# Kernel tuning notes

Hardware: AMD Instinct MI355X
Metric: run time of the kernel (lower is better)

## Reference

```python
import math
import jax, jax.numpy as jnp
import numpy as np

DEPTH, EMB, HEADS = 6, 768, 12
B, N = 2, 2048
LN_EPS = 1e-6


def _get_attention_slopes(n):
    def p2(n):
        start = 2 ** (-2 ** (-(math.log2(n) - 3)))
        return [start * start ** i for i in range(n)]
    if math.log2(n).is_integer():
        return p2(n)
    c = 2 ** math.floor(math.log2(n))
    return p2(c) + _get_attention_slopes(2 * c)[0::2][: n - c]


def layer_norm(x, scale, bias):
    m = jnp.mean(x, axis=-1, keepdims=True)
    v = jnp.var(x, axis=-1, keepdims=True)
    return (x - m) * jax.lax.rsqrt(v + LN_EPS) * scale + bias


def setup_inputs() -> dict:
    key = jax.random.key(0)
    ks = jax.random.split(key, 6)
    s = 0.02
    return {
        "x": jax.random.normal(ks[0], (B, N, EMB), jnp.float32),
        "wqkv": jax.random.normal(ks[1], (DEPTH, EMB, 3 * EMB), jnp.float32) * s,
        "bqkv": jnp.zeros((DEPTH, 3 * EMB), jnp.float32),
        "wo": jax.random.normal(ks[2], (DEPTH, EMB, EMB), jnp.float32) * s,
        "bo": jnp.zeros((DEPTH, EMB), jnp.float32),
        "ln1s": jnp.ones((DEPTH, EMB), jnp.float32),
        "ln1b": jnp.zeros((DEPTH, EMB), jnp.float32),
        "ln2s": jnp.ones((DEPTH, EMB), jnp.float32),
        "ln2b": jnp.zeros((DEPTH, EMB), jnp.float32),
        "w1": jax.random.normal(ks[3], (DEPTH, EMB, 4 * EMB), jnp.float32) * s,
        "w2": jax.random.normal(ks[4], (DEPTH, 4 * EMB, EMB), jnp.float32) * s,
        "lnfs": jnp.ones((EMB,), jnp.float32),
        "lnfb": jnp.zeros((EMB,), jnp.float32),
    }


def reference(x, wqkv, bqkv, wo, bo, ln1s, ln1b, ln2s, ln2b, w1, w2, lnfs, lnfb):
    Bx, n, E = x.shape
    H = HEADS
    Dh = E // H
    scale = Dh ** -0.5
    slopes = jnp.asarray(_get_attention_slopes(H), dtype=x.dtype)  # [H]
    # ALiBi-style bias: slope[h] * key-position (absolute), per source code
    pos_bias = slopes[:, None, None] * jnp.arange(n, dtype=x.dtype)[None, None, :]  # [H,1,n]
    causal = jnp.tril(jnp.ones((n, n), bool))
    big_neg = jnp.finfo(x.dtype).min

    def block(h, p):
        Wqkv, Bqkv, Wo, Bo, L1s, L1b, L2s, L2b, W1, W2 = p
        y = layer_norm(h, L1s, L1b)
        qkv = y @ Wqkv + Bqkv  # [B,n,3E]
        q, k, v = jnp.split(qkv, 3, axis=-1)
        mh = lambda t: t.reshape(Bx, n, H, Dh).transpose(0, 2, 1, 3)  # b h n d
        q, k, v = mh(q), mh(k), mh(v)
        att = jnp.einsum("bhnd,bhmd->bhnm", q, k) * scale + pos_bias[None]
        att = jnp.where(causal, att, big_neg)
        att = jax.nn.softmax(att, axis=-1)
        o = jnp.einsum("bhnm,bhmd->bhnd", att, v)
        o = o.transpose(0, 2, 1, 3).reshape(Bx, n, E) @ Wo + Bo
        h = h + o
        y = layer_norm(h, L2s, L2b)
        y = jax.nn.gelu(y @ W1) @ W2  # fc1 (no bias) -> gelu -> fc2 (no bias)
        return h + y, None

    h, _ = jax.lax.scan(block, x, (wqkv, bqkv, wo, bo, ln1s, ln1b, ln2s, ln2b, w1, w2))
    return layer_norm(h, lnfs, lnfb)
```

## Files before the change

### kernel.cpp

```cpp
#include <hip/hip_runtime.h>
#include <hip/hip_bf16.h>
#include <stdint.h>


typedef __bf16 bf16_t;
typedef __bf16 bf16x8 __attribute__((ext_vector_type(8)));
typedef __bf16 bf16x4 __attribute__((ext_vector_type(4)));
typedef float f32x4 __attribute__((ext_vector_type(4)));

#define EMB   768
#define NSEQ  2048
#define BATCH 2
#define NHEAD 12
#define NDEPTH 6
#define MROWS (BATCH * NSEQ)

__constant__ float c_slopes[NHEAD] = {
    0.5f, 0.25f, 0.125f, 0.0625f, 0.03125f, 0.015625f, 0.0078125f, 0.00390625f,
    0.7071067811865476f, 0.3535533905932738f, 0.1767766952966369f, 0.08838834764831845f};

__global__ void detect_kernel(const void* __restrict__ lnfs, int* __restrict__ flag) {
  if (threadIdx.x == 0 && blockIdx.x == 0) {
    uint32_t u = *(const uint32_t*)lnfs;
    *flag = (u == 0x3F800000u) ? 0 : 1;
  }
}

__global__ void fill_one_kernel(bf16_t* __restrict__ o, int n) {
  int i = blockIdx.x * blockDim.x + threadIdx.x;
  if (i < n) o[i] = (bf16_t)1.0f;
}

__global__ void cast_kernel(const void* __restrict__ x_, float* __restrict__ h, int n,
                            const int* __restrict__ flagp) {
  const int flag = *flagp;
  int i = blockIdx.x * blockDim.x + threadIdx.x;
  if (i < n) h[i] = flag ? (float)((const bf16_t*)x_)[i] : ((const float*)x_)[i];
}

template <int FINAL>
__global__ __launch_bounds__(256) void ln_kernel(const float* __restrict__ x,
                                                 const void* __restrict__ sc_,
                                                 const void* __restrict__ bi_,
                                                 size_t eoff, void* __restrict__ y_,
                                                 const int* __restrict__ flagp) {
  const int flag = *flagp;
  const int widx = blockIdx.x * 4 + (threadIdx.x >> 6);
  const int lane = threadIdx.x & 63;
  const float* row = x + (size_t)widx * EMB;
  float v[12];
  float sum = 0.f, ss = 0.f;
#pragma unroll
  for (int i = 0; i < 12; ++i) {
    float t = row[lane + i * 64];
    v[i] = t; sum += t; ss += t * t;
  }
#pragma unroll
  for (int m = 1; m < 64; m <<= 1) {
    sum += __shfl_xor(sum, m, 64);
    ss  += __shfl_xor(ss, m, 64);
  }
  const float mean = sum * (1.f / 768.f);
  const float var  = ss * (1.f / 768.f) - mean * mean;
  const float rs   = rsqrtf(var + 1e-6f);
#pragma unroll
  for (int i = 0; i < 12; ++i) {
    const int d = lane + i * 64;
    const float s = flag ? (float)((const bf16_t*)sc_)[eoff + d] : ((const float*)sc_)[eoff + d];
    const float b = flag ? (float)((const bf16_t*)bi_)[eoff + d] : ((const float*)bi_)[eoff + d];
    const float o = (v[i] - mean) * rs * s + b;
    if (FINAL == 0 || flag) ((bf16_t*)y_)[(size_t)widx * EMB + d] = (bf16_t)o;
    else                    ((float*)y_)[(size_t)widx * EMB + d] = o;
  }
}

__global__ __launch_bounds__(256) void transpose_k(const void* __restrict__ W_, size_t eoff,
                                                   bf16_t* __restrict__ T, int R, int C,
                                                   const int* __restrict__ flagp) {
  __shared__ bf16_t tile[64][72];
  const int c0 = blockIdx.x * 64, r0 = blockIdx.y * 64;
  const int t = threadIdx.x;
  if (*flagp) {
    const bf16_t* W = (const bf16_t*)W_ + eoff;
#pragma unroll
    for (int k = 0; k < 2; ++k) {
      int idx = t + k * 256;
      int r = idx >> 3, s = idx & 7;
      *(bf16x8*)&tile[r][s * 8] = *(const bf16x8*)(W + (size_t)(r0 + r) * C + c0 + s * 8);
    }
  } else {
    const float* W = (const float*)W_ + eoff;
#pragma unroll
    for (int q = 0; q < 16; ++q) {
      int idx = t + q * 256;
      int r = idx >> 6, c = idx & 63;
      tile[r][c] = (bf16_t)W[(size_t)(r0 + r) * C + c0 + c];
    }
  }
  __syncthreads();
#pragma unroll
  for (int k = 0; k < 2; ++k) {
    int idx = t + k * 256;
    int orow = idx >> 3, s = idx & 7;
    bf16x8 v;
#pragma unroll
    for (int q = 0; q < 8; ++q) v[q] = tile[s * 8 + q][orow];
    *(bf16x8*)(T + (size_t)(c0 + orow) * R + r0 + s * 8) = v;
  }
}

__device__ __forceinline__ float gelu_f(float x) {
  float u = 0.7978845608028654f * (x + 0.044715f * x * x * x);
  float t = tanhf(u);
  return 0.5f * x * (1.0f + t);
}

template <int MODE>
__global__ __launch_bounds__(256) void gemm_bt(const bf16_t* __restrict__ A,
                                               const bf16_t* __restrict__ Bt,
                                               const void* __restrict__ bias_, size_t boff,
                                               bf16_t* __restrict__ out,
                                               float* __restrict__ hio, int N, int K,
                                               const int* __restrict__ flagp) {
  __shared__ bf16_t Als[128 * 32];
  __shared__ bf16_t Bls[128 * 32];
  const int flag = *flagp;
  const int tid = threadIdx.x;
  const int wave = tid >> 6, lane = tid & 63;
  const int bm = blockIdx.y * 128, bn = blockIdx.x * 128;
  const int kc = blockIdx.z;
  const int Kc = K / (int)gridDim.z;
  const int kbeg = kc * Kc, kend = kbeg + Kc;
  const int wm = (wave >> 1) * 64, wn = (wave & 1) * 64;
  const int rl = lane & 15, quad = lane >> 4;

  f32x4 acc[4][4];
#pragma unroll
  for (int i = 0; i < 4; ++i)
#pragma unroll
    for (int j = 0; j < 4; ++j) acc[i][j] = (f32x4){0.f, 0.f, 0.f, 0.f};

  const int tr0 = wave * 32 + (lane >> 2);
  const int tc  = (lane & 3) * 8;

  for (int k0 = kbeg; k0 < kend; k0 += 32) {
#pragma unroll
    for (int j = 0; j < 2; ++j) {
      const int tr = tr0 + j * 16;
      bf16x8 av = *(const bf16x8*)(A  + (size_t)(bm + tr) * K + k0 + tc);
      bf16x8 bv = *(const bf16x8*)(Bt + (size_t)(bn + tr) * K + k0 + tc);
      *(bf16x8*)&Als[tr * 32 + tc] = av;
      *(bf16x8*)&Bls[tr * 32 + tc] = bv;
    }
    __syncthreads();
    bf16x8 af[4], bfv[4];
#pragma unroll
    for (int i = 0; i < 4; ++i) af[i] = *(const bf16x8*)&Als[(wm + i * 16 + rl) * 32 + quad * 8];
#pragma unroll
    for (int j = 0; j < 4; ++j) bfv[j] = *(const bf16x8*)&Bls[(wn + j * 16 + rl) * 32 + quad * 8];
#pragma unroll
    for (int i = 0; i < 4; ++i)
#pragma unroll
      for (int j = 0; j < 4; ++j)
        acc[i][j] = __builtin_amdgcn_mfma_f32_16x16x32_bf16(af[i], bfv[j], acc[i][j], 0, 0, 0);
    __syncthreads();
  }

  const int r0 = bm + wm + quad * 4;
  const int cb = bn + wn + rl;
#pragma unroll
  for (int j = 0; j < 4; ++j) {
    const int c = cb + j * 16;
    const float bv = (bias_ && kc == 0)
                         ? (flag ? (float)((const bf16_t*)bias_)[boff + c]
                                 : ((const float*)bias_)[boff + c])
                         : 0.f;
#pragma unroll
    for (int i = 0; i < 4; ++i) {
      const int rbase = r0 + i * 16;
      f32x4 a = acc[i][j];
#pragma unroll
      for (int rr = 0; rr < 4; ++rr) {
        const float v = a[rr] + bv;
        const size_t idx = (size_t)(rbase + rr) * N + c;
        if (MODE == 0) out[idx] = (bf16_t)v;
        else if (MODE == 1) out[idx] = (bf16_t)gelu_f(v);
        else atomicAdd(&hio[idx], v);
      }
    }
  }
}

__global__ __launch_bounds__(256) void gemm_qkv(const bf16_t* __restrict__ A,
                                                const bf16_t* __restrict__ Bt,
                                                const void* __restrict__ bias_, size_t boff,
                                                bf16_t* __restrict__ Qb,
                                                bf16_t* __restrict__ Kpk,
                                                bf16_t* __restrict__ Vtp,
                                                const int* __restrict__ flagp) {
  constexpr int N = 3 * EMB, K = EMB;
  __shared__ bf16_t Als[128 * 32];
  __shared__ bf16_t Bls[128 * 32];
  const int flag = *flagp;
  const int tid = threadIdx.x;
  const int wave = tid >> 6, lane = tid & 63;
  const int bm = blockIdx.y * 128, bn = blockIdx.x * 128;
  const int wm = (wave >> 1) * 64, wn = (wave & 1) * 64;
  const int rl = lane & 15, quad = lane >> 4;

  f32x4 acc[4][4];
#pragma unroll
  for (int i = 0; i < 4; ++i)
#pragma unroll
    for (int j = 0; j < 4; ++j) acc[i][j] = (f32x4){0.f, 0.f, 0.f, 0.f};

  const int tr0 = wave * 32 + (lane >> 2);
  const int tc  = (lane & 3) * 8;

  for (int k0 = 0; k0 < K; k0 += 32) {
#pragma unroll
    for (int j = 0; j < 2; ++j) {
      const int tr = tr0 + j * 16;
      bf16x8 av  = *(const bf16x8*)(A  + (size_t)(bm + tr) * K + k0 + tc);
      bf16x8 bvv = *(const bf16x8*)(Bt + (size_t)(bn + tr) * K + k0 + tc);
      *(bf16x8*)&Als[tr * 32 + tc] = av;
      *(bf16x8*)&Bls[tr * 32 + tc] = bvv;
    }
    __syncthreads();
    bf16x8 af[4], bfv[4];
#pragma unroll
    for (int i = 0; i < 4; ++i) af[i] = *(const bf16x8*)&Als[(wm + i * 16 + rl) * 32 + quad * 8];
#pragma unroll
    for (int j = 0; j < 4; ++j) bfv[j] = *(const bf16x8*)&Bls[(wn + j * 16 + rl) * 32 + quad * 8];
#pragma unroll
    for (int i = 0; i < 4; ++i)
#pragma unroll
      for (int j = 0; j < 4; ++j)
        acc[i][j] = __builtin_amdgcn_mfma_f32_16x16x32_bf16(af[i], bfv[j], acc[i][j], 0, 0, 0);
    __syncthreads();
  }

  const int r0 = bm + wm + quad * 4;
  const int cb = bn + wn + rl;
  const int seg = bn / EMB;
#pragma unroll
  for (int j = 0; j < 4; ++j) {
    const int c = cb + j * 16;
    const float bv = flag ? (float)((const bf16_t*)bias_)[boff + c]
                          : ((const float*)bias_)[boff + c];
    const int cc = c - seg * EMB;
    const int hh = cc >> 6, d = cc & 63;
#pragma unroll
    for (int i = 0; i < 4; ++i) {
      const int rbase = r0 + i * 16;
      const int bb = rbase >> 11, n0 = rbase & 2047;
      f32x4 a = acc[i][j];
      if (seg == 0) {
#pragma unroll
        for (int rr = 0; rr < 4; ++rr)
          Qb[(size_t)(rbase + rr) * EMB + cc] = (bf16_t)(a[rr] + bv);
      } else if (seg == 1) {
        const size_t kidx = ((size_t)(bb * NHEAD + hh) * NSEQ + n0) * 64 + d;
#pragma unroll
        for (int rr = 0; rr < 4; ++rr)
          Kpk[kidx + (size_t)rr * 64] = (bf16_t)(a[rr] + bv);
      } else {
        bf16x4 pk;
#pragma unroll
        for (int rr = 0; rr < 4; ++rr) pk[rr] = (bf16_t)(a[rr] + bv);
        *(bf16x4*)&Vtp[((size_t)(bb * NHEAD + hh) * 64 + d) * NSEQ + n0] = pk;
      }
    }
  }
}

__global__ __launch_bounds__(128) void attn_flash(const bf16_t* __restrict__ Qb,
                                                  const bf16_t* __restrict__ Kpk,
                                                  const bf16_t* __restrict__ Vtp,
                                                  bf16_t* __restrict__ o) {
  __shared__ bf16_t Kls[2][32][72];
  __shared__ bf16_t Vls[2][64][40];
  __shared__ bf16_t Pls[2][16][40];
  const int tid = threadIdx.x;
  const int wave = tid >> 6, lane = tid & 63;
  const int qt = 63 - (int)blockIdx.x;
  const int bh = blockIdx.y;
  const int h = bh % NHEAD, b = bh / NHEAD;
  const float slope = c_slopes[h];
  const int q0 = qt * 32 + wave * 16;
  const int rl = lane & 15, quad = lane >> 4;

  const bf16_t* qbase = Qb + (size_t)(b * NSEQ + q0 + rl) * EMB + h * 64;
  const bf16x8 qf0 = *(const bf16x8*)(qbase + quad * 8);
  const bf16x8 qf1 = *(const bf16x8*)(qbase + 32 + quad * 8);

  const bf16_t* kg = Kpk + (size_t)bh * NSEQ * 64;
  const bf16_t* vg = Vtp + (size_t)bh * 64 * NSEQ;

  f32x4 acc[4];
#pragma unroll
  for (int db = 0; db < 4; ++db) acc[db] = (f32x4){0.f, 0.f, 0.f, 0.f};
  float lsum = 0.f;

  const int skey = tid >> 2, sc = (tid & 3) * 16;
  const int vdim = tid >> 1, vk = (tid & 1) * 16;
  const int vswz = (vdim >> 3) & 3;
  const int vo0 = (((vk >> 3) + 0) ^ vswz) * 8;
  const int vo1 = (((vk >> 3) + 1) ^ vswz) * 8;

  const float mq = slope * (float)(q0 + rl);
  float aoff[2][4];
#pragma unroll
  for (int f = 0; f < 2; ++f)
#pragma unroll
    for (int r = 0; r < 4; ++r)
      aoff[f][r] = slope * (float)(f * 16 + quad * 4 + r) - mq;

  const int pswz = (rl >> 2) & 3;
  const int pbase0 = (((quad >> 1) + 0) ^ pswz) * 8 + (quad & 1) * 4;
  const int pbase1 = (((quad >> 1) + 2) ^ pswz) * 8 + (quad & 1) * 4;

  const int ntiles = qt + 1;
  bf16x8 kr0, kr1, vr0, vr1;
  {
    const bf16_t* kp_ = kg + (size_t)skey * 64 + sc;
    kr0 = *(const bf16x8*)kp_;
    kr1 = *(const bf16x8*)(kp_ + 8);
    const bf16_t* vp_ = vg + (size_t)vdim * NSEQ + vk;
    vr0 = *(const bf16x8*)vp_;
    vr1 = *(const bf16x8*)(vp_ + 8);
  }

  for (int t = 0; t < ntiles; ++t) {
    const int p = t & 1;
    const int kb = t * 32;
    *(bf16x8*)&Kls[p][skey][sc]     = kr0;
    *(bf16x8*)&Kls[p][skey][sc + 8] = kr1;
    *(bf16x8*)&Vls[p][vdim][vo0]    = vr0;
    *(bf16x8*)&Vls[p][vdim][vo1]    = vr1;
    __syncthreads();
    if (t + 1 < ntiles) {
      const bf16_t* kp_ = kg + (size_t)(kb + 32 + skey) * 64 + sc;
      kr0 = *(const bf16x8*)kp_;
      kr1 = *(const bf16x8*)(kp_ + 8);
      const bf16_t* vp_ = vg + (size_t)vdim * NSEQ + kb + 32 + vk;
      vr0 = *(const bf16x8*)vp_;
      vr1 = *(const bf16x8*)(vp_ + 8);
    }

    f32x4 s2[2];
#pragma unroll
    for (int f = 0; f < 2; ++f) {
      const bf16x8 kf0 = *(const bf16x8*)&Kls[p][f * 16 + rl][quad * 8];
      const bf16x8 kf1 = *(const bf16x8*)&Kls[p][f * 16 + rl][32 + quad * 8];
      f32x4 z = (f32x4){0.f, 0.f, 0.f, 0.f};
      z = __builtin_amdgcn_mfma_f32_16x16x32_bf16(kf0, qf0, z, 0, 0, 0);
      z = __builtin_amdgcn_mfma_f32_16x16x32_bf16(kf1, qf1, z, 0, 0, 0);
      s2[f] = z;
    }

    const bool full = (kb + 31 <= q0);
    const float kbase = slope * (float)kb;
    bf16x4 pk0, pk1;
#pragma unroll
    for (int f = 0; f < 2; ++f) {
#pragma unroll
      for (int r = 0; r < 4; ++r) {
        const int key = kb + f * 16 + quad * 4 + r;
        const bool valid = full || (key <= q0 + rl);
        const float e = valid ? __expf(fmaf(s2[f][r], 0.125f, kbase + aoff[f][r])) : 0.f;
        lsum += e;
        if (f == 0) pk0[r] = (bf16_t)e;
        else        pk1[r] = (bf16_t)e;
      }
    }
    *(bf16x4*)&Pls[wave][rl][pbase0] = pk0;
    *(bf16x4*)&Pls[wave][rl][pbase1] = pk1;

    const bf16x8 pf = *(const bf16x8*)&Pls[wave][rl][(quad ^ pswz) * 8];
#pragma unroll
    for (int db = 0; db < 4; ++db) {
      const int dim = db * 16 + rl;
      const bf16x8 vf = *(const bf16x8*)&Vls[p][dim][(quad ^ ((dim >> 3) & 3)) * 8];
      acc[db] = __builtin_amdgcn_mfma_f32_16x16x32_bf16(pf, vf, acc[db], 0, 0, 0);
    }
  }

  float lt = lsum;
  lt += __shfl_xor(lt, 16, 64);
  lt += __shfl_xor(lt, 32, 64);
#pragma unroll
  for (int r = 0; r < 4; ++r) {
    const float linv = 1.f / __shfl(lt, quad * 4 + r, 64);
    const size_t rowo = (size_t)(b * NSEQ + q0 + quad * 4 + r) * EMB + h * 64;
#pragma unroll
    for (int db = 0; db < 4; ++db)
      o[rowo + db * 16 + rl] = (bf16_t)(acc[db][r] * linv);
  }
}

extern "C" void kernel_launch(void* const* d_in, const int* in_sizes, int n_in,
                              void* d_out, int out_size, void* d_ws, size_t ws_size,
                              hipStream_t stream) {
  const void* x    = d_in[0];
  const void* wqkv = d_in[1];
  const void* bqkv = d_in[2];
  const void* wo   = d_in[3];
  const void* bo   = d_in[4];
  const void* ln1s = d_in[5];
  const void* ln1b = d_in[6];
  const void* ln2s = d_in[7];
  const void* ln2b = d_in[8];
  const void* w1   = d_in[9];
  const void* w2   = d_in[10];
  const void* lnfs = d_in[11];
  const void* lnfb = d_in[12];

  const size_t need = 12582912ull + 6291456ull + 25165824ull + 4718592ull + 256ull;
  if (ws_size < need) {
    fill_one_kernel<<<(out_size + 255) / 256, 256, 0, stream>>>((bf16_t*)d_out, out_size);
    return;
  }

  char* p = (char*)d_ws;
  float*  h  = (float*)p;  p += 12582912ull;
  bf16_t* y  = (bf16_t*)p; p += 6291456ull;
  bf16_t* u  = (bf16_t*)p; p += 25165824ull;
  bf16_t* wT = (bf16_t*)p; p += 4718592ull;
  int* flagp = (int*)p;
  bf16_t* Qb   = u;
  bf16_t* Kpk  = u + 3145728;
  bf16_t* Vtp  = u + 6291456;
  bf16_t* t1   = u;
  bf16_t* attno = y;

  detect_kernel<<<1, 64, 0, stream>>>(lnfs, flagp);
  cast_kernel<<<(MROWS * EMB) / 256, 256, 0, stream>>>(x, h, MROWS * EMB, flagp);

  for (int l = 0; l < NDEPTH; ++l) {
    const size_t sE   = (size_t)l * EMB;
    const size_t s3E  = (size_t)l * 3 * EMB;
    const size_t wq_o = (size_t)l * EMB * 3 * EMB;
    const size_t wo_o = (size_t)l * EMB * EMB;
    const size_t w1_o = (size_t)l * EMB * 4 * EMB;

    ln_kernel<0><<<MROWS / 4, 256, 0, stream>>>(h, ln1s, ln1b, sE, y, flagp);
    transpose_k<<<dim3(36, 12), 256, 0, stream>>>(wqkv, wq_o, wT, 768, 2304, flagp);
    gemm_qkv<<<dim3(18, 32), 256, 0, stream>>>(y, wT, bqkv, s3E, Qb, Kpk, Vtp, flagp);
    attn_flash<<<dim3(64, BATCH * NHEAD), 128, 0, stream>>>(Qb, Kpk, Vtp, attno);
    transpose_k<<<dim3(12, 12), 256, 0, stream>>>(wo, wo_o, wT, 768, 768, flagp);
    gemm_bt<2><<<dim3(6, 32, 4), 256, 0, stream>>>(attno, wT, bo, sE, nullptr, h,
                                                   EMB, EMB, flagp);
    ln_kernel<0><<<MROWS / 4, 256, 0, stream>>>(h, ln2s, ln2b, sE, y, flagp);
    transpose_k<<<dim3(48, 12), 256, 0, stream>>>(w1, w1_o, wT, 768, 3072, flagp);
    gemm_bt<1><<<dim3(24, 32), 256, 0, stream>>>(y, wT, nullptr, 0, t1, nullptr,
                                                 4 * EMB, EMB, flagp);
    transpose_k<<<dim3(12, 48), 256, 0, stream>>>(w2, w1_o, wT, 3072, 768, flagp);
    gemm_bt<2><<<dim3(6, 32, 4), 256, 0, stream>>>(t1, wT, nullptr, 0, nullptr, h,
                                                   EMB, 4 * EMB, flagp);
  }
  ln_kernel<1><<<MROWS / 4, 256, 0, stream>>>(h, lnfs, lnfb, 0, d_out, flagp);
}
```

Measured before the change: 1.986 ms.

## Load K/V fragments directly from global into registers in flash attention

Removes the shared-memory staging of K and V tiles, and with it the per-tile __syncthreads. Each wave now loads its MFMA operand fragments straight from global memory into registers and prefetches the next tile's K and V. It also adds s_setprio around the MFMA groups and splits the row-sum accumulator into two. The trade-off is that both waves of a block now load the same K/V tile separately, doubling global/L2 traffic, and the fragment loads are less coalesced than the old cooperative loads.

```diff
diff --git a/kernel.cpp b/kernel.cpp
--- a/kernel.cpp
+++ b/kernel.cpp
@@ -278,8 +278,6 @@
                                                   const bf16_t* __restrict__ Kpk,
                                                   const bf16_t* __restrict__ Vtp,
                                                   bf16_t* __restrict__ o) {
-  __shared__ bf16_t Kls[2][32][72];
-  __shared__ bf16_t Vls[2][64][40];
   __shared__ bf16_t Pls[2][16][40];
   const int tid = threadIdx.x;
   const int wave = tid >> 6, lane = tid & 63;
@@ -294,19 +292,13 @@
   const bf16x8 qf0 = *(const bf16x8*)(qbase + quad * 8);
   const bf16x8 qf1 = *(const bf16x8*)(qbase + 32 + quad * 8);
 
-  const bf16_t* kg = Kpk + (size_t)bh * NSEQ * 64;
-  const bf16_t* vg = Vtp + (size_t)bh * 64 * NSEQ;
+  const bf16_t* kp0 = Kpk + (size_t)bh * NSEQ * 64 + (size_t)rl * 64 + quad * 8;
+  const bf16_t* vp0 = Vtp + (size_t)bh * 64 * NSEQ + (size_t)rl * NSEQ + quad * 8;
 
   f32x4 acc[4];
 #pragma unroll
   for (int db = 0; db < 4; ++db) acc[db] = (f32x4){0.f, 0.f, 0.f, 0.f};
-  float lsum = 0.f;
-
-  const int skey = tid >> 2, sc = (tid & 3) * 16;
-  const int vdim = tid >> 1, vk = (tid & 1) * 16;
-  const int vswz = (vdim >> 3) & 3;
-  const int vo0 = (((vk >> 3) + 0) ^ vswz) * 8;
-  const int vo1 = (((vk >> 3) + 1) ^ vswz) * 8;
+  float lsum0 = 0.f, lsum1 = 0.f;
 
   const float mq = slope * (float)(q0 + rl);
   float aoff[2][4];
@@ -321,72 +313,78 @@
   const int pbase1 = (((quad >> 1) + 2) ^ pswz) * 8 + (quad & 1) * 4;
 
   const int ntiles = qt + 1;
-  bf16x8 kr0, kr1, vr0, vr1;
-  {
-    const bf16_t* kp_ = kg + (size_t)skey * 64 + sc;
-    kr0 = *(const bf16x8*)kp_;
-    kr1 = *(const bf16x8*)(kp_ + 8);
-    const bf16_t* vp_ = vg + (size_t)vdim * NSEQ + vk;
-    vr0 = *(const bf16x8*)vp_;
-    vr1 = *(const bf16x8*)(vp_ + 8);
-  }
+  bf16x8 kr0 = *(const bf16x8*)(kp0);
+  bf16x8 kr1 = *(const bf16x8*)(kp0 + 32);
+  bf16x8 kr2 = *(const bf16x8*)(kp0 + 16 * 64);
+  bf16x8 kr3 = *(const bf16x8*)(kp0 + 16 * 64 + 32);
+  bf16x8 vr0 = *(const bf16x8*)(vp0);
+  bf16x8 vr1 = *(const bf16x8*)(vp0 + 16 * NSEQ);
+  bf16x8 vr2 = *(const bf16x8*)(vp0 + 32 * NSEQ);
+  bf16x8 vr3 = *(const bf16x8*)(vp0 + 48 * NSEQ);
 
   for (int t = 0; t < ntiles; ++t) {
-    const int p = t & 1;
     const int kb = t * 32;
-    *(bf16x8*)&Kls[p][skey][sc]     = kr0;
-    *(bf16x8*)&Kls[p][skey][sc + 8] = kr1;
-    *(bf16x8*)&Vls[p][vdim][vo0]    = vr0;
-    *(bf16x8*)&Vls[p][vdim][vo1]    = vr1;
-    __syncthreads();
+
+    f32x4 s2[2];
+    __builtin_amdgcn_s_setprio(1);
+    {
+      f32x4 z = (f32x4){0.f, 0.f, 0.f, 0.f};
+      z = __builtin_amdgcn_mfma_f32_16x16x32_bf16(kr0, qf0, z, 0, 0, 0);
+      z = __builtin_amdgcn_mfma_f32_16x16x32_bf16(kr1, qf1, z, 0, 0, 0);
+      s2[0] = z;
+      z = (f32x4){0.f, 0.f, 0.f, 0.f};
+      z = __builtin_amdgcn_mfma_f32_16x16x32_bf16(kr2, qf0, z, 0, 0, 0);
+      z = __builtin_amdgcn_mfma_f32_16x16x32_bf16(kr3, qf1, z, 0, 0, 0);
+      s2[1] = z;
+    }
+    __builtin_amdgcn_s_setprio(0);
     if (t + 1 < ntiles) {
-      const bf16_t* kp_ = kg + (size_t)(kb + 32 + skey) * 64 + sc;
-      kr0 = *(const bf16x8*)kp_;
-      kr1 = *(const bf16x8*)(kp_ + 8);
-      const bf16_t* vp_ = vg + (size_t)vdim * NSEQ + kb + 32 + vk;
-      vr0 = *(const bf16x8*)vp_;
-      vr1 = *(const bf16x8*)(vp_ + 8);
-    }
-
-    f32x4 s2[2];
-#pragma unroll
-    for (int f = 0; f < 2; ++f) {
-      const bf16x8 kf0 = *(const bf16x8*)&Kls[p][f * 16 + rl][quad * 8];
-      const bf16x8 kf1 = *(const bf16x8*)&Kls[p][f * 16 + rl][32 + quad * 8];
-      f32x4 z = (f32x4){0.f, 0.f, 0.f, 0.f};
-      z = __builtin_amdgcn_mfma_f32_16x16x32_bf16(kf0, qf0, z, 0, 0, 0);
-      z = __builtin_amdgcn_mfma_f32_16x16x32_bf16(kf1, qf1, z, 0, 0, 0);
-      s2[f] = z;
+      const bf16_t* kp = kp0 + (size_t)(kb + 32) * 64;
+      kr0 = *(const bf16x8*)(kp);
+      kr1 = *(const bf16x8*)(kp + 32);
+      kr2 = *(const bf16x8*)(kp + 16 * 64);
+      kr3 = *(const bf16x8*)(kp + 16 * 64 + 32);
     }
 
     const bool full = (kb + 31 <= q0);
     const float kbase = slope * (float)kb;
     bf16x4 pk0, pk1;
 #pragma unroll
-    for (int f = 0; f < 2; ++f) {
-#pragma unroll
-      for (int r = 0; r < 4; ++r) {
-        const int key = kb + f * 16 + quad * 4 + r;
-        const bool valid = full || (key <= q0 + rl);
-        const float e = valid ? __expf(fmaf(s2[f][r], 0.125f, kbase + aoff[f][r])) : 0.f;
-        lsum += e;
-        if (f == 0) pk0[r] = (bf16_t)e;
-        else        pk1[r] = (bf16_t)e;
-      }
+    for (int r = 0; r < 4; ++r) {
+      const int key = kb + quad * 4 + r;
+      const bool valid = full || (key <= q0 + rl);
+      const float e = valid ? __expf(fmaf(s2[0][r], 0.125f, kbase + aoff[0][r])) : 0.f;
+      lsum0 += e;
+      pk0[r] = (bf16_t)e;
+    }
+#pragma unroll
+    for (int r = 0; r < 4; ++r) {
+      const int key = kb + 16 + quad * 4 + r;
+      const bool valid = full || (key <= q0 + rl);
+      const float e = valid ? __expf(fmaf(s2[1][r], 0.125f, kbase + aoff[1][r])) : 0.f;
+      lsum1 += e;
+      pk1[r] = (bf16_t)e;
     }
     *(bf16x4*)&Pls[wave][rl][pbase0] = pk0;
     *(bf16x4*)&Pls[wave][rl][pbase1] = pk1;
 
     const bf16x8 pf = *(const bf16x8*)&Pls[wave][rl][(quad ^ pswz) * 8];
-#pragma unroll
-    for (int db = 0; db < 4; ++db) {
-      const int dim = db * 16 + rl;
-      const bf16x8 vf = *(const bf16x8*)&Vls[p][dim][(quad ^ ((dim >> 3) & 3)) * 8];
-      acc[db] = __builtin_amdgcn_mfma_f32_16x16x32_bf16(pf, vf, acc[db], 0, 0, 0);
-    }
-  }
-
-  float lt = lsum;
+    __builtin_amdgcn_s_setprio(1);
+    acc[0] = __builtin_amdgcn_mfma_f32_16x16x32_bf16(pf, vr0, acc[0], 0, 0, 0);
+    acc[1] = __builtin_amdgcn_mfma_f32_16x16x32_bf16(pf, vr1, acc[1], 0, 0, 0);
+    acc[2] = __builtin_amdgcn_mfma_f32_16x16x32_bf16(pf, vr2, acc[2], 0, 0, 0);
+    acc[3] = __builtin_amdgcn_mfma_f32_16x16x32_bf16(pf, vr3, acc[3], 0, 0, 0);
+    __builtin_amdgcn_s_setprio(0);
+    if (t + 1 < ntiles) {
+      const bf16_t* vp = vp0 + kb + 32;
+      vr0 = *(const bf16x8*)(vp);
+      vr1 = *(const bf16x8*)(vp + 16 * NSEQ);
+      vr2 = *(const bf16x8*)(vp + 32 * NSEQ);
+      vr3 = *(const bf16x8*)(vp + 48 * NSEQ);
+    }
+  }
+
+  float lt = lsum0 + lsum1;
   lt += __shfl_xor(lt, 16, 64);
   lt += __shfl_xor(lt, 32, 64);
 #pragma unroll
```

New measurement: 2.585 ms. +30.2%, slower.
